# Kernel tuning notes

Measured on AMD Instinct MI355X. Metric: run time of the kernel, lower is better.

The kernel has to match this reference:

```python
import jax, jax.numpy as jnp
import numpy as np

# Static config (matches init_kwargs / input_specs)
B, P, A, D, K = 8, 1, 8, 8, 3          # batch, num_plans, action_channels, dim_qk, receptive_field
T, H, W = 32, 32, 32                   # 3D grid
PAD = K // 2
PA = P * A
PAD_VALUE = 0.0


def _pad3(t, val=PAD_VALUE):
    # pad last three (spatial) dims by PAD on each side
    return jnp.pad(t, ((0, 0), (0, 0), (PAD, PAD), (PAD, PAD), (PAD, PAD)), constant_values=val)


def _conv3d(x, w):
    # x: [B, Ci, T, H, W], w: [Co, Ci, K, K, K], VALID padding (input pre-padded)
    return jax.lax.conv_general_dilated(
        x, w, window_strides=(1, 1, 1), padding='VALID',
        dimension_numbers=('NCDHW', 'OIDHW', 'NCDHW'))


def setup_inputs() -> dict:
    key = jax.random.key(0)
    k1, k2, k3, k4 = jax.random.split(key, 4)
    s = 1.0 / np.sqrt(P * K ** 3)  # conv fan-in init scale
    return {
        'values':  jax.random.normal(k1, (B, P, T, H, W), jnp.float32),
        'rewards': jax.random.normal(k2, (B, P, T, H, W), jnp.float32),
        'w_qk':    jax.random.normal(k3, (2 * PA * D, P, K, K, K), jnp.float32) * s,
        'w_v':     jax.random.normal(k4, (PA, P, K, K, K), jnp.float32) * s,
    }


def reference(values, rewards, w_qk, w_v):
    x = values + rewards                       # [B, P, T, H, W]
    xp = _pad3(x)

    qk = _conv3d(xp, w_qk)                     # [B, 2*PA*D, T, H, W]
    q, k = jnp.split(qk, 2, axis=1)            # each [B, PA*D, T, H, W]

    # softmax value-conv weights over the flattened 3D kernel per (out, in) pair
    wv = jax.nn.softmax(w_v.reshape(PA, P, K ** 3), axis=-1).reshape(w_v.shape)
    v = _conv3d(xp, wv)                        # [B, PA, T, H, W]

    kp, vp = _pad3(k), _pad3(v)
    thw = T * H * W
    qf = q.reshape(B, PA, D, thw)              # [B, A, D, thw]

    # local 3x3x3 neighborhood attention: per kernel offset, dot q with shifted k
    # (same math as unfoldNd + einsum, without the K^3*D memory blow-up)
    sims, vns = [], []
    for dt in range(K):
        for dh in range(K):
            for dw in range(K):
                ksh = jax.lax.slice(kp, (0, 0, dt, dh, dw),
                                    (B, PA * D, dt + T, dh + H, dw + W)).reshape(B, PA, D, thw)
                sims.append(jnp.einsum('badt,badt->bat', qf, ksh))
                vns.append(jax.lax.slice(vp, (0, 0, dt, dh, dw),
                                         (B, PA, dt + T, dh + H, dw + W)).reshape(B, PA, thw))

    sim = jnp.stack(sims, axis=-1)             # [B, A, thw, K^3]
    attn = jax.nn.softmax(sim, axis=-1)
    vn = jnp.stack(vns, axis=2)                # [B, A, K^3, thw]
    q_values = jnp.einsum('batn,bant->bat', attn, vn)  # [B, A, thw]

    q_values = q_values.reshape(B, P, A, T, H, W)
    # ActionSelector with soft_maxpool=False: hard max over actions
    next_values = jnp.max(q_values, axis=2)    # [B, P, T, H, W]
    return next_values
```

## Files before the change

### kernel.cpp

```cpp
#include <hip/hip_runtime.h>
#include <hip/hip_bf16.h>

#define NB   8
#define NA   8
#define ND   8
#define NCH  64
#define GT   32
#define KREG 216
#define IMS  40

#define XS_OFF   0
#define BTS_OFF  2048
#define IMC_OFF  13568
#define KV_OFF   0
#define QS_OFF   31104
#define POOL_SZ  40320

typedef _Float16 h2_t  __attribute__((ext_vector_type(2)));
typedef _Float16 f16x8 __attribute__((ext_vector_type(8)));
typedef float    f32x4 __attribute__((ext_vector_type(4)));

static __device__ __forceinline__ unsigned pack_h2(float a, float b) {
#if __has_builtin(__builtin_amdgcn_cvt_pkrtz)
    return __builtin_bit_cast(unsigned, __builtin_amdgcn_cvt_pkrtz(a, b));
#else
    unsigned short ha = __builtin_bit_cast(unsigned short, (_Float16)a);
    unsigned short hb = __builtin_bit_cast(unsigned short, (_Float16)b);
    return (unsigned)ha | ((unsigned)hb << 16);
#endif
}

static __device__ __forceinline__ float dot2(unsigned k, unsigned q, float c) {
#if __has_builtin(__builtin_amdgcn_fdot2)
    return __builtin_amdgcn_fdot2(__builtin_bit_cast(h2_t, k),
                                  __builtin_bit_cast(h2_t, q), c, false);
#else
    h2_t a = __builtin_bit_cast(h2_t, k), b = __builtin_bit_cast(h2_t, q);
    return c + (float)a[0] * (float)b[0] + (float)a[1] * (float)b[1];
#endif
}

__global__ void prep_weights(const float* __restrict__ w_qk,
                             const float* __restrict__ w_v,
                             unsigned* __restrict__ ws) {
    int t = threadIdx.x;
    if (t >= 144) return;
    float r[28];
    r[27] = 0.f;
    if (t < 64) {
        const float* w = w_qk + (NCH + t) * 27;
        #pragma unroll
        for (int j = 0; j < 27; ++j) r[j] = w[j];
    } else if (t < 72) {
        int a = t - 64;
        float m = -1e30f;
        #pragma unroll
        for (int j = 0; j < 27; ++j) { r[j] = w_v[a * 27 + j]; m = fmaxf(m, r[j]); }
        float s = 0.f;
        #pragma unroll
        for (int j = 0; j < 27; ++j) { r[j] = __expf(r[j] - m); s += r[j]; }
        float inv = 1.f / s;
        #pragma unroll
        for (int j = 0; j < 27; ++j) r[j] *= inv;
    } else if (t < 80) {
        #pragma unroll
        for (int j = 0; j < 27; ++j) r[j] = 0.f;
    } else {
        const float* w = w_qk + (t - 80) * 27;
        const float L2E = 1.44269504f;
        #pragma unroll
        for (int j = 0; j < 27; ++j) r[j] = w[j] * L2E;
    }
    unsigned* dst = ws + t * (IMS / 2);
    #pragma unroll
    for (int p = 0; p < 14; ++p) dst[p] = pack_h2(r[2 * p], r[2 * p + 1]);
    #pragma unroll
    for (int p = 14; p < 20; ++p) dst[p] = 0u;
}

__launch_bounds__(256, 4)
__global__ void avi_kernel(const float* __restrict__ values,
                           const float* __restrict__ rewards,
                           const unsigned* __restrict__ wsBTS,
                           float* __restrict__ out) {
    __shared__ __align__(16) char pool[POOL_SZ];
    float*    xS   = (float*)(pool + XS_OFF);
    _Float16* BTSl = (_Float16*)(pool + BTS_OFF);
    _Float16* imc  = (_Float16*)(pool + IMC_OFF);
    char*     kvS  = pool + KV_OFF;
    char*     qS   = pool + QS_OFF;

    const int tid  = threadIdx.x;
    const int bb   = blockIdx.x >> 9;
    const int tile = blockIdx.x & 511;
    const int tz = tile >> 6, ty = (tile >> 3) & 7, tx = tile & 7;
    const int g0z = tz * 4, g0y = ty * 4, g0x = tx * 4;
    const int base_in = bb * (GT * GT * GT);

    for (int i = tid; i < 512; i += 256) {
        int lz = i >> 6, ly = (i >> 3) & 7, lx = i & 7;
        int gz = g0z + lz - 2, gy = g0y + ly - 2, gx = g0x + lx - 2;
        float v = 0.f;
        if ((unsigned)gz < 32u && (unsigned)gy < 32u && (unsigned)gx < 32u) {
            int idx = base_in + gz * 1024 + gy * 32 + gx;
            v = values[idx] + rewards[idx];
        }
        xS[i] = v;
    }
    for (int i = tid; i < 720; i += 256)
        ((int4*)BTSl)[i] = ((const int4*)wsBTS)[i];
    __syncthreads();

    if (tid < 224) {
        unsigned rowU[16];
        if (tid < KREG) {
            int vz = tid / 36, rem = tid - vz * 36, vy = rem / 6, vx = rem - vy * 6;
            int gz = g0z + vz - 1, gy = g0y + vy - 1, gx = g0x + vx - 1;
            float mask = ((unsigned)gz < 32u && (unsigned)gy < 32u && (unsigned)gx < 32u)
                             ? 1.f : 0.f;
            float xr[27];
            #pragma unroll
            for (int t = 0; t < 27; ++t) {
                int dz = t / 9, dy = (t / 3) % 3, dx = t % 3;
                xr[t] = xS[(vz + dz) * 64 + (vy + dy) * 8 + (vx + dx)] * mask;
            }
            #pragma unroll
            for (int p = 0; p < 13; ++p) rowU[p] = pack_h2(xr[2 * p], xr[2 * p + 1]);
            rowU[13] = pack_h2(xr[26], 0.f);
            rowU[14] = rowU[15] = 0u;
        } else {
            #pragma unroll
            for (int p = 0; p < 16; ++p) rowU[p] = 0u;
        }
        int4* dst = (int4*)((char*)imc + tid * (IMS * 2));
        dst[0] = make_int4(rowU[0], rowU[1], rowU[2], rowU[3]);
        dst[1] = make_int4(rowU[4], rowU[5], rowU[6], rowU[7]);
        dst[2] = make_int4(rowU[8], rowU[9], rowU[10], rowU[11]);
        dst[3] = make_int4(rowU[12], rowU[13], rowU[14], rowU[15]);
    }

    const int lane = tid & 63;
    const int wave = tid >> 6;
    const int quad = lane >> 4;
    const int l15  = lane & 15;

    f16x8 af[9];
    #pragma unroll
    for (int mt = 0; mt < 9; ++mt)
        af[mt] = *(const f16x8*)(BTSl + (mt * 16 + l15) * IMS + quad * 8);

    __syncthreads();

    f16x8 bf[4];
    #pragma unroll
    for (int i = 0; i < 4; ++i) {
        int nt = wave + i * 4;
        if (nt < 14)
            bf[i] = *(const f16x8*)(imc + (nt * 16 + l15) * IMS + quad * 8);
    }

    __syncthreads();

    for (int i = 0; i < 4; ++i) {
        int nt = wave + i * 4;
        if (nt >= 14) break;
        int n = nt * 16 + l15;
        bool nvalid = (n < KREG);
        int vz = n / 36, rm = n - vz * 36, vy = rm / 6, vx = rm - vy * 6;
        bool ctr = ((unsigned)(vz - 1) < 4u) && ((unsigned)(vy - 1) < 4u) &&
                   ((unsigned)(vx - 1) < 4u);
        int cvox = (vz - 1) * 16 + (vy - 1) * 4 + (vx - 1);
        char* rowB = kvS + n * 144;
        char* rowQ = qS + cvox * 144;
        #pragma unroll
        for (int mt = 0; mt < 9; ++mt) {
            f32x4 d = __builtin_amdgcn_mfma_f32_16x16x32_f16(
                af[mt], bf[i], (f32x4){0.f, 0.f, 0.f, 0.f}, 0, 0, 0);
            if (mt < 4) {
                if (nvalid) {
                    int2 w2;
                    w2.x = (int)pack_h2(d[0], d[1]);
                    w2.y = (int)pack_h2(d[2], d[3]);
                    *(int2*)(rowB + (mt * 16 + quad * 4) * 2) = w2;
                }
            } else if (mt == 4) {
                if (nvalid && quad < 2) {
                    int2 w2;
                    w2.x = (int)pack_h2(d[0], d[1]);
                    w2.y = (int)pack_h2(d[2], d[3]);
                    *(int2*)(rowB + 128 + quad * 8) = w2;
                }
            } else {
                if (ctr) {
                    int ch0 = (mt - 5) * 16 + quad * 4;
                    int a = ch0 >> 3, d0 = ch0 & 7;
                    int2 w2;
                    w2.x = (int)pack_h2(d[0], d[1]);
                    w2.y = (int)pack_h2(d[2], d[3]);
                    *(int2*)(rowQ + a * 16 + d0 * 2) = w2;
                }
            }
        }
    }
    __syncthreads();

    const int clz = lane >> 4, cly = (lane >> 2) & 3, clx = lane & 3;
    const int rbase = clz * 36 + cly * 6 + clx;

    float best = -1e30f;
    #pragma unroll
    for (int ti = 0; ti < 2; ++ti) {
        int a = wave + ti * 4;
        const int4 qv = *(const int4*)(qS + lane * 144 + a * 16);
        unsigned qp[4] = {(unsigned)qv.x, (unsigned)qv.y,
                          (unsigned)qv.z, (unsigned)qv.w};
        float ssum = 0.f, acc = 0.f;
        #pragma unroll
        for (int nn = 0; nn < 27; ++nn) {
            int dz = nn / 9, dy = (nn / 3) % 3, dx = nn % 3;
            int r = rbase + dz * 36 + dy * 6 + dx;
            const char* rowB = kvS + r * 144;
            const int4 kr = *(const int4*)(rowB + a * 16);
            float s = dot2((unsigned)kr.x, qp[0],
                      dot2((unsigned)kr.y, qp[1],
                      dot2((unsigned)kr.z, qp[2],
                      dot2((unsigned)kr.w, qp[3], 0.f))));
            float e = exp2f(s);
            float fv = (float)*(const _Float16*)(rowB + 128 + a * 2);
            ssum += e;
            acc = fmaf(e, fv, acc);
        }
        best = fmaxf(best, acc / ssum);
    }
    *(float*)(qS + lane * 144 + 128 + wave * 4) = best;
    __syncthreads();

    if (tid < 64) {
        float4 p = *(const float4*)(qS + tid * 144 + 128);
        float mx = fmaxf(fmaxf(p.x, p.y), fmaxf(p.z, p.w));
        int lz2 = tid >> 4, ly2 = (tid >> 2) & 3, lx2 = tid & 3;
        int o = base_in + (g0z + lz2) * 1024 + (g0y + ly2) * 32 + (g0x + lx2);
        out[o] = mx;
    }
}

extern "C" void kernel_launch(void* const* d_in, const int* in_sizes, int n_in,
                              void* d_out, int out_size, void* d_ws, size_t ws_size,
                              hipStream_t stream) {
    const float* values  = (const float*)d_in[0];
    const float* rewards = (const float*)d_in[1];
    const float* w_qk    = (const float*)d_in[2];
    const float* w_v     = (const float*)d_in[3];
    unsigned* ws = (unsigned*)d_ws;

    prep_weights<<<1, 256, 0, stream>>>(w_qk, w_v, ws);
    avi_kernel<<<NB * 512, 256, 0, stream>>>(values, rewards, ws,
                                             (float*)d_out);
}
```

Before: 109.5 us.

## Fuse weight prep into main kernel and interleave two action attention loops

Removes the separate single-block prep_weights launch: each block now reads w_qk/w_v from global memory, applies the softmax and log2e scaling itself, and writes the packed fp16 weights straight into shared memory. This drops one launch and the dependency between two kernels, but every one of the 4096 blocks repeats the weight prep and its global reads. The attention loop also processes both actions of a wave in one 27-iteration loop, loading the value row once as an int4 and extracting the halves. This gives more independent work per iteration to hide latency, at some register cost.

After: 127.2 us. +16.2%, slower.

```diff
diff --git a/kernel.cpp b/kernel.cpp
--- a/kernel.cpp
+++ b/kernel.cpp
@@ -40,48 +40,11 @@
 #endif
 }
 
-__global__ void prep_weights(const float* __restrict__ w_qk,
-                             const float* __restrict__ w_v,
-                             unsigned* __restrict__ ws) {
-    int t = threadIdx.x;
-    if (t >= 144) return;
-    float r[28];
-    r[27] = 0.f;
-    if (t < 64) {
-        const float* w = w_qk + (NCH + t) * 27;
-        #pragma unroll
-        for (int j = 0; j < 27; ++j) r[j] = w[j];
-    } else if (t < 72) {
-        int a = t - 64;
-        float m = -1e30f;
-        #pragma unroll
-        for (int j = 0; j < 27; ++j) { r[j] = w_v[a * 27 + j]; m = fmaxf(m, r[j]); }
-        float s = 0.f;
-        #pragma unroll
-        for (int j = 0; j < 27; ++j) { r[j] = __expf(r[j] - m); s += r[j]; }
-        float inv = 1.f / s;
-        #pragma unroll
-        for (int j = 0; j < 27; ++j) r[j] *= inv;
-    } else if (t < 80) {
-        #pragma unroll
-        for (int j = 0; j < 27; ++j) r[j] = 0.f;
-    } else {
-        const float* w = w_qk + (t - 80) * 27;
-        const float L2E = 1.44269504f;
-        #pragma unroll
-        for (int j = 0; j < 27; ++j) r[j] = w[j] * L2E;
-    }
-    unsigned* dst = ws + t * (IMS / 2);
-    #pragma unroll
-    for (int p = 0; p < 14; ++p) dst[p] = pack_h2(r[2 * p], r[2 * p + 1]);
-    #pragma unroll
-    for (int p = 14; p < 20; ++p) dst[p] = 0u;
-}
-
 __launch_bounds__(256, 4)
 __global__ void avi_kernel(const float* __restrict__ values,
                            const float* __restrict__ rewards,
-                           const unsigned* __restrict__ wsBTS,
+                           const float* __restrict__ w_qk,
+                           const float* __restrict__ w_v,
                            float* __restrict__ out) {
     __shared__ __align__(16) char pool[POOL_SZ];
     float*    xS   = (float*)(pool + XS_OFF);
@@ -107,8 +70,39 @@
         }
         xS[i] = v;
     }
-    for (int i = tid; i < 720; i += 256)
-        ((int4*)BTSl)[i] = ((const int4*)wsBTS)[i];
+    if (tid < 144) {
+        float r[28];
+        r[27] = 0.f;
+        if (tid < 64) {
+            const float* w = w_qk + (NCH + tid) * 27;
+            #pragma unroll
+            for (int j = 0; j < 27; ++j) r[j] = w[j];
+        } else if (tid < 72) {
+            int a = tid - 64;
+            float m = -1e30f;
+            #pragma unroll
+            for (int j = 0; j < 27; ++j) { r[j] = w_v[a * 27 + j]; m = fmaxf(m, r[j]); }
+            float s = 0.f;
+            #pragma unroll
+            for (int j = 0; j < 27; ++j) { r[j] = __expf(r[j] - m); s += r[j]; }
+            float inv = 1.f / s;
+            #pragma unroll
+            for (int j = 0; j < 27; ++j) r[j] *= inv;
+        } else if (tid < 80) {
+            #pragma unroll
+            for (int j = 0; j < 27; ++j) r[j] = 0.f;
+        } else {
+            const float* w = w_qk + (tid - 80) * 27;
+            const float L2E = 1.44269504f;
+            #pragma unroll
+            for (int j = 0; j < 27; ++j) r[j] = w[j] * L2E;
+        }
+        unsigned* dst = (unsigned*)(BTSl + tid * IMS);
+        #pragma unroll
+        for (int p = 0; p < 14; ++p) dst[p] = pack_h2(r[2 * p], r[2 * p + 1]);
+        #pragma unroll
+        for (int p = 14; p < 20; ++p) dst[p] = 0u;
+    }
     __syncthreads();
 
     if (tid < 224) {
@@ -206,32 +200,45 @@
 
     const int clz = lane >> 4, cly = (lane >> 2) & 3, clx = lane & 3;
     const int rbase = clz * 36 + cly * 6 + clx;
-
-    float best = -1e30f;
+    const int a0 = wave, a1 = wave + 4;
+    const unsigned vsh = (wave & 1) * 16;
+
+    const int4 qv0 = *(const int4*)(qS + lane * 144 + a0 * 16);
+    const int4 qv1 = *(const int4*)(qS + lane * 144 + a1 * 16);
+    unsigned qp0[4] = {(unsigned)qv0.x, (unsigned)qv0.y,
+                       (unsigned)qv0.z, (unsigned)qv0.w};
+    unsigned qp1[4] = {(unsigned)qv1.x, (unsigned)qv1.y,
+                       (unsigned)qv1.z, (unsigned)qv1.w};
+
+    float ssum0 = 0.f, acc0 = 0.f, ssum1 = 0.f, acc1 = 0.f;
     #pragma unroll
-    for (int ti = 0; ti < 2; ++ti) {
-        int a = wave + ti * 4;
-        const int4 qv = *(const int4*)(qS + lane * 144 + a * 16);
-        unsigned qp[4] = {(unsigned)qv.x, (unsigned)qv.y,
-                          (unsigned)qv.z, (unsigned)qv.w};
-        float ssum = 0.f, acc = 0.f;
-        #pragma unroll
-        for (int nn = 0; nn < 27; ++nn) {
-            int dz = nn / 9, dy = (nn / 3) % 3, dx = nn % 3;
-            int r = rbase + dz * 36 + dy * 6 + dx;
-            const char* rowB = kvS + r * 144;
-            const int4 kr = *(const int4*)(rowB + a * 16);
-            float s = dot2((unsigned)kr.x, qp[0],
-                      dot2((unsigned)kr.y, qp[1],
-                      dot2((unsigned)kr.z, qp[2],
-                      dot2((unsigned)kr.w, qp[3], 0.f))));
-            float e = exp2f(s);
-            float fv = (float)*(const _Float16*)(rowB + 128 + a * 2);
-            ssum += e;
-            acc = fmaf(e, fv, acc);
-        }
-        best = fmaxf(best, acc / ssum);
-    }
+    for (int nn = 0; nn < 27; ++nn) {
+        int dz = nn / 9, dy = (nn / 3) % 3, dx = nn % 3;
+        int r = rbase + dz * 36 + dy * 6 + dx;
+        const char* rowB = kvS + r * 144;
+        const int4 k0 = *(const int4*)(rowB + a0 * 16);
+        const int4 k1 = *(const int4*)(rowB + a1 * 16);
+        const int4 vu = *(const int4*)(rowB + 128);
+        float s0 = dot2((unsigned)k0.x, qp0[0],
+                   dot2((unsigned)k0.y, qp0[1],
+                   dot2((unsigned)k0.z, qp0[2],
+                   dot2((unsigned)k0.w, qp0[3], 0.f))));
+        float s1 = dot2((unsigned)k1.x, qp1[0],
+                   dot2((unsigned)k1.y, qp1[1],
+                   dot2((unsigned)k1.z, qp1[2],
+                   dot2((unsigned)k1.w, qp1[3], 0.f))));
+        float e0 = exp2f(s0);
+        float e1 = exp2f(s1);
+        unsigned hw0 = ((const unsigned*)&vu)[wave >> 1];
+        unsigned hw1 = ((const unsigned*)&vu)[(wave >> 1) + 2];
+        float v0 = (float)__builtin_bit_cast(_Float16,
+                       (unsigned short)((hw0 >> vsh) & 0xffffu));
+        float v1 = (float)__builtin_bit_cast(_Float16,
+                       (unsigned short)((hw1 >> vsh) & 0xffffu));
+        ssum0 += e0; acc0 = fmaf(e0, v0, acc0);
+        ssum1 += e1; acc1 = fmaf(e1, v1, acc1);
+    }
+    float best = fmaxf(acc0 / ssum0, acc1 / ssum1);
     *(float*)(qS + lane * 144 + 128 + wave * 4) = best;
     __syncthreads();
 
@@ -251,9 +258,6 @@
     const float* rewards = (const float*)d_in[1];
     const float* w_qk    = (const float*)d_in[2];
     const float* w_v     = (const float*)d_in[3];
-    unsigned* ws = (unsigned*)d_ws;
-
-    prep_weights<<<1, 256, 0, stream>>>(w_qk, w_v, ws);
-    avi_kernel<<<NB * 512, 256, 0, stream>>>(values, rewards, ws,
+    avi_kernel<<<NB * 512, 256, 0, stream>>>(values, rewards, w_qk, w_v,
                                              (float*)d_out);
 }
```
